# Kernel optimization log

Measured on AMD Instinct MI355X. Metric: run time of the kernel, lower is better.

## Reference

```python
import jax, jax.numpy as jnp
import numpy as np


def _apply_ry(state, theta, i, n):
    # state: [B, 2^n] complex; theta: scalar or [B]
    B = state.shape[0]
    s = state.reshape(B, 2**i, 2, 2**(n - i - 1))
    th = jnp.reshape(theta, (-1, 1, 1)) * 0.5
    c, sn = jnp.cos(th), jnp.sin(th)
    a0, a1 = s[:, :, 0], s[:, :, 1]
    return jnp.stack([c * a0 - sn * a1, sn * a0 + c * a1], axis=2).reshape(B, -1)


def _apply_rz(state, theta, i, n):
    B = state.shape[0]
    s = state.reshape(B, 2**i, 2, 2**(n - i - 1))
    ph = jnp.exp(-0.5j * jnp.reshape(theta, (-1, 1, 1)).astype(jnp.float32))
    return jnp.stack([s[:, :, 0] * ph, s[:, :, 1] * jnp.conj(ph)], axis=2).reshape(B, -1)


def _apply_cnot(state, c, t, n):
    # CNOT(control=c, target=t); flips target amplitudes on control=1 slice
    B = state.shape[0]
    s = state.reshape((B,) + (2,) * n)
    ax_c, ax_t = 1 + c, 1 + t
    zero = jnp.take(s, 0, axis=ax_c)
    one = jnp.take(s, 1, axis=ax_c)
    one = jnp.flip(one, axis=ax_t - (1 if t > c else 0))
    return jnp.stack([zero, one], axis=ax_c).reshape(B, -1)


def _z_signs(n):
    # signs[i, k] = +1 if bit i of basis index k is 0 else -1 (qubit 0 = MSB)
    idx = np.arange(2**n)
    bits = (idx[None, :] >> (n - 1 - np.arange(n))[:, None]) & 1
    return jnp.asarray(1.0 - 2.0 * bits, dtype=jnp.float32)  # [n, 2^n]


def _circuit(q_in, w_ry, w_rz):
    # Batched state-vector simulation of: AngleEmbedding(RY) ->
    # n_layers x (per-qubit RY,RZ + CNOT ring) -> <Z_i> expectations.
    B, n = q_in.shape
    L = w_ry.shape[0]
    state = jnp.zeros((B, 2**n), jnp.complex64).at[:, 0].set(1.0)
    for i in range(n):  # AngleEmbedding with rotation='Y'
        state = _apply_ry(state, q_in[:, i], i, n)
    for l in range(L):
        for i in range(n):
            state = _apply_ry(state, w_ry[l, i], i, n)
            state = _apply_rz(state, w_rz[l, i], i, n)
        for i in range(n):  # CNOT ring
            state = _apply_cnot(state, i, (i + 1) % n, n)
    probs = jnp.abs(state) ** 2  # [B, 2^n]
    return probs @ _z_signs(n).T  # [B, n] = <Z_i>


def setup_inputs():
    key = jax.random.key(0)
    ks = jax.random.split(key, 6)
    B, D, n, L = 4096, 512, 10, 4
    return {
        "x": jax.random.normal(ks[0], (B, D), jnp.float32),
        "pre_w": jax.random.normal(ks[1], (n, D), jnp.float32) / np.sqrt(D).astype(np.float32),
        "pre_b": jnp.zeros((n,), jnp.float32),
        "post_w": jax.random.normal(ks[2], (1, n), jnp.float32) / np.sqrt(n).astype(np.float32),
        "post_b": jnp.zeros((1,), jnp.float32),
        "w_ry": jax.random.normal(ks[3], (L, n), jnp.float32),
        "w_rz": jax.random.normal(ks[4], (L, n), jnp.float32),
    }


def reference(x, pre_w, pre_b, post_w, post_b, w_ry, w_rz):
    q_in = x @ pre_w.T + pre_b      # pre_net: [B, n_qubits] rotation angles
    z = _circuit(q_in, w_ry, w_rz)  # [B, n_qubits] PauliZ expectations
    return z @ post_w.T + post_b    # post_net: [B, 1] logits
```

## Files before the change

### kernel.cpp

```cpp
#include <hip/hip_runtime.h>

#define DEV static __device__ __forceinline__

template <int CTRL>
DEV float dpp_mov(float v) {
    int i = __float_as_int(v);
    i = __builtin_amdgcn_update_dpp(i, i, CTRL, 0xF, 0xF, false);
    return __int_as_float(i);
}
template <int PAT>
DEV float swz(float v) {
    return __int_as_float(__builtin_amdgcn_ds_swizzle(__float_as_int(v), PAT));
}
DEV float bperm(int byteaddr, float v) {
    return __int_as_float(__builtin_amdgcn_ds_bpermute(byteaddr, __float_as_int(v)));
}

#if __has_builtin(__builtin_amdgcn_permlane16_swap)
#define HAVE_PL16 1
DEV void pl16_pair(float v, float &r0, float &r1) {
    auto r = __builtin_amdgcn_permlane16_swap(__float_as_int(v), __float_as_int(v),
                                              false, false);
    r0 = __int_as_float((int)r[0]);
    r1 = __int_as_float((int)r[1]);
}
#endif
#if __has_builtin(__builtin_amdgcn_permlane32_swap)
#define HAVE_PL32 1
DEV void pl32_pair(float v, float &r0, float &r1) {
    auto r = __builtin_amdgcn_permlane32_swap(__float_as_int(v), __float_as_int(v),
                                              false, false);
    r0 = __int_as_float((int)r[0]);
    r1 = __int_as_float((int)r[1]);
}
#endif

DEV float wave_sum(float v, int a32) {
    v += dpp_mov<0xB1>(v);
    v += dpp_mov<0x4E>(v);
    v += dpp_mov<0x141>(v);
    v += dpp_mov<0x128>(v);
#ifdef HAVE_PL16
    {
        float r0, r1;
        pl16_pair(v, r0, r1);
        v = r0 + r1;
    }
#else
    v += swz<0x401F>(v);
#endif
#ifdef HAVE_PL32
    {
        float r0, r1;
        pl32_pair(v, r0, r1);
        v = r0 + r1;
    }
#else
    v += bperm(a32, v);
#endif
    return v;
}

template <int P>
DEV void apply_ry(float (&re)[16], float (&im)[16], float c, float s, int lane,
                  int a32, bool cv16, bool cv32) {
    if constexpr (P == 9) {
#ifdef HAVE_PL32
        const bool hi = (lane & 32) != 0;
        const float fl = hi ? s : c;
        const float fh = hi ? c : -s;
        const float g0 = cv32 ? fl : fh;
        const float g1 = cv32 ? fh : fl;
#pragma unroll
        for (int r = 0; r < 16; ++r) {
            float x0, x1, y0, y1;
            pl32_pair(re[r], x0, x1);
            pl32_pair(im[r], y0, y1);
            re[r] = fmaf(g0, x0, g1 * x1);
            im[r] = fmaf(g0, y0, g1 * y1);
        }
#else
        const float sg = (lane & 32) ? s : -s;
#pragma unroll
        for (int r = 0; r < 16; ++r) {
            float pr = bperm(a32, re[r]);
            float pi = bperm(a32, im[r]);
            re[r] = fmaf(c, re[r], sg * pr);
            im[r] = fmaf(c, im[r], sg * pi);
        }
#endif
    } else if constexpr (P == 8) {
#ifdef HAVE_PL16
        const bool hi = (lane & 16) != 0;
        const float fl = hi ? s : c;
        const float fh = hi ? c : -s;
        const float g0 = cv16 ? fl : fh;
        const float g1 = cv16 ? fh : fl;
#pragma unroll
        for (int r = 0; r < 16; ++r) {
            float x0, x1, y0, y1;
            pl16_pair(re[r], x0, x1);
            pl16_pair(im[r], y0, y1);
            re[r] = fmaf(g0, x0, g1 * x1);
            im[r] = fmaf(g0, y0, g1 * y1);
        }
#else
        const float sg = (lane & 16) ? s : -s;
#pragma unroll
        for (int r = 0; r < 16; ++r) {
            float pr = swz<0x401F>(re[r]);
            float pi = swz<0x401F>(im[r]);
            re[r] = fmaf(c, re[r], sg * pr);
            im[r] = fmaf(c, im[r], sg * pi);
        }
#endif
    } else if constexpr (P >= 4) {
        constexpr int mask = 1 << (P - 4);
        const float sg = (lane & mask) ? s : -s;
#pragma unroll
        for (int r = 0; r < 16; ++r) {
            float pr, pi;
            if constexpr (mask == 8) {
                pr = dpp_mov<0x128>(re[r]);
                pi = dpp_mov<0x128>(im[r]);
            } else if constexpr (mask == 4) {
                pr = dpp_mov<0x1B>(dpp_mov<0x141>(re[r]));
                pi = dpp_mov<0x1B>(dpp_mov<0x141>(im[r]));
            } else if constexpr (mask == 2) {
                pr = dpp_mov<0x4E>(re[r]);
                pi = dpp_mov<0x4E>(im[r]);
            } else {
                pr = dpp_mov<0xB1>(re[r]);
                pi = dpp_mov<0xB1>(im[r]);
            }
            re[r] = fmaf(c, re[r], sg * pr);
            im[r] = fmaf(c, im[r], sg * pi);
        }
    } else {
        constexpr int tb = 1 << P;
#pragma unroll
        for (int r = 0; r < 16; ++r) {
            if (!(r & tb)) {
                const int r2 = r | tb;
                float a0r = re[r], a1r = re[r2];
                float a0i = im[r], a1i = im[r2];
                re[r]  = fmaf(c, a0r, -s * a1r);
                re[r2] = fmaf(s, a0r,  c * a1r);
                im[r]  = fmaf(c, a0i, -s * a1i);
                im[r2] = fmaf(s, a0i,  c * a1i);
            }
        }
    }
}

DEV int g_of(int a) {
    a ^= ((a >> 1) & 1) ? 1 : 0;
    a ^= ((a >> 2) & 1) ? 2 : 0;
    a ^= ((a >> 3) & 1) ? 4 : 0;
    a ^= ((a >> 4) & 1) ? 8 : 0;
    a ^= ((a >> 5) & 1) ? 16 : 0;
    return a;
}

DEV void build_rz_tables(const float (&zc)[10], const float (&zs)[10], int lane,
                         float (&p67r)[4], float (&p67i)[4], float (&p89r)[4],
                         float (&p89i)[4]) {
    float plr, pli;
    pli = ((lane >> 5) & 1) ? zs[0] : -zs[0];
    plr = zc[0];
#pragma unroll
    for (int q = 1; q < 6; ++q) {
        float sq = ((lane >> (5 - q)) & 1) ? zs[q] : -zs[q];
        float nr = plr * zc[q] - pli * sq;
        float ni = plr * sq + pli * zc[q];
        plr = nr; pli = ni;
    }
    const float c6 = zc[6], s6 = zs[6], c7 = zc[7], s7 = zs[7];
    const float c8 = zc[8], s8 = zs[8], c9 = zc[9], s9 = zs[9];
#pragma unroll
    for (int j = 0; j < 4; ++j) {
        float sg6 = (j >> 1) ? s6 : -s6;
        float sg7 = (j & 1) ? s7 : -s7;
        float ar = c6 * c7 - sg6 * sg7;
        float ai = c6 * sg7 + sg6 * c7;
        p67r[j] = ar * plr - ai * pli;
        p67i[j] = ar * pli + ai * plr;
        float sg8 = (j >> 1) ? s8 : -s8;
        float sg9 = (j & 1) ? s9 : -s9;
        p89r[j] = c8 * c9 - sg8 * sg9;
        p89i[j] = c8 * sg9 + sg8 * c9;
    }
}

DEV void cnot_ring(float (&re)[16], float (&im)[16], int cA, int cB, int lane) {
#pragma unroll
    for (int r = 0; r < 16; ++r) {
        const int addr = ((0x6996 >> r) & 1) ? cB : cA;
        re[r] = bperm(addr, re[r]);
        im[r] = bperm(addr, im[r]);
    }
    {
        const bool ctrl = (lane & 1) != 0;
#pragma unroll
        for (int r = 0; r < 8; ++r) {
            const int r2 = r | 8;
            float t0 = re[r], t1 = re[r2];
            re[r]  = ctrl ? t1 : t0;
            re[r2] = ctrl ? t0 : t1;
            float u0 = im[r], u1 = im[r2];
            im[r]  = ctrl ? u1 : u0;
            im[r2] = ctrl ? u0 : u1;
        }
    }
#pragma unroll
    for (int r = 0; r < 16; ++r)
        if ((r & 8) && !(r & 4)) {
            const int r2 = r | 4;
            float t = re[r]; re[r] = re[r2]; re[r2] = t;
            t = im[r]; im[r] = im[r2]; im[r2] = t;
        }
#pragma unroll
    for (int r = 0; r < 16; ++r)
        if ((r & 4) && !(r & 2)) {
            const int r2 = r | 2;
            float t = re[r]; re[r] = re[r2]; re[r2] = t;
            t = im[r]; im[r] = im[r2]; im[r2] = t;
        }
#pragma unroll
    for (int r = 0; r < 16; ++r)
        if ((r & 2) && !(r & 1)) {
            const int r2 = r | 1;
            float t = re[r]; re[r] = re[r2]; re[r2] = t;
            t = im[r]; im[r] = im[r2]; im[r2] = t;
        }
}

__global__ __launch_bounds__(256, 4) void dqc_main_kernel(
    const float* __restrict__ x, const float* __restrict__ pre_w,
    const float* __restrict__ pre_b, const float* __restrict__ post_w,
    const float* __restrict__ post_b, const float* __restrict__ w_ry,
    const float* __restrict__ w_rz, float* __restrict__ out, int B) {
    __shared__ float2 sh_trig[80];
    {
        int t = threadIdx.x;
        if (t < 80) {
            float ang = (t < 40 ? w_ry[t] : w_rz[t - 40]) * 0.5f;
            float sv, cv;
            __sincosf(ang, &sv, &cv);
            sh_trig[t] = make_float2(cv, sv);
        }
    }
    __syncthreads();

    const int lane = threadIdx.x & 63;
    const int wid = threadIdx.x >> 6;
    const int b = blockIdx.x * 4 + wid;
    if (b >= B) return;

    const int a32 = (lane ^ 32) << 2;

    bool cv16 = false, cv32 = false;
#ifdef HAVE_PL16
    {
        auto r = __builtin_amdgcn_permlane16_swap(lane, lane, false, false);
        cv16 = ((int)r[0] == (lane & ~16));
    }
#endif
#ifdef HAVE_PL32
    {
        auto r = __builtin_amdgcn_permlane32_swap(lane, lane, false, false);
        cv32 = ((int)r[0] == (lane & ~32));
    }
#endif

    const int h0 = lane ^ ((lane & 1) ? 32 : 0);
    const int cA = g_of(h0) << 2;
    const int cB = g_of(h0 ^ 32) << 2;

    float th[10];
#pragma unroll
    for (int i = 0; i < 10; ++i) th[i] = 0.f;
    const float4* xb4 = reinterpret_cast<const float4*>(x + (size_t)b * 512);
    const float4* pw4 = reinterpret_cast<const float4*>(pre_w);
#pragma unroll
    for (int k = 0; k < 2; ++k) {
        const int idx = lane + 64 * k;
        const float4 xv = xb4[idx];
#pragma unroll
        for (int i = 0; i < 10; ++i) {
            const float4 wv = pw4[i * 128 + idx];
            th[i] = fmaf(xv.x, wv.x, th[i]);
            th[i] = fmaf(xv.y, wv.y, th[i]);
            th[i] = fmaf(xv.z, wv.z, th[i]);
            th[i] = fmaf(xv.w, wv.w, th[i]);
        }
    }
#pragma unroll
    for (int i = 0; i < 10; ++i) th[i] = wave_sum(th[i], a32) + pre_b[i];

    float f0r[10], f0i[10], f1r[10], f1i[10];
#pragma unroll
    for (int q = 0; q < 10; ++q) {
        float hh = 0.5f * (th[q] + w_ry[q]);
        float sh_, ch_;
        __sincosf(hh, &sh_, &ch_);
        float2 z = sh_trig[40 + q];
        f0r[q] = ch_ * z.x;  f0i[q] = -ch_ * z.y;
        f1r[q] = sh_ * z.x;  f1i[q] =  sh_ * z.y;
    }
    float Lr, Li;
    {
        int bq = (lane >> 5) & 1;
        Lr = bq ? f1r[0] : f0r[0];
        Li = bq ? f1i[0] : f0i[0];
#pragma unroll
        for (int q = 1; q < 6; ++q) {
            int bb = (lane >> (5 - q)) & 1;
            float br = bb ? f1r[q] : f0r[q];
            float bi = bb ? f1i[q] : f0i[q];
            float nr = Lr * br - Li * bi;
            float ni = Lr * bi + Li * br;
            Lr = nr; Li = ni;
        }
    }
    float t67r[4], t67i[4], t89r[4], t89i[4];
#pragma unroll
    for (int j = 0; j < 4; ++j) {
        float ar = (j >> 1) ? f1r[6] : f0r[6];
        float ai = (j >> 1) ? f1i[6] : f0i[6];
        float br = (j & 1) ? f1r[7] : f0r[7];
        float bi = (j & 1) ? f1i[7] : f0i[7];
        float pr = ar * br - ai * bi;
        float pi = ar * bi + ai * br;
        t67r[j] = pr * Lr - pi * Li;
        t67i[j] = pr * Li + pi * Lr;
        float cr_ = (j >> 1) ? f1r[8] : f0r[8];
        float ci_ = (j >> 1) ? f1i[8] : f0i[8];
        float dr = (j & 1) ? f1r[9] : f0r[9];
        float di = (j & 1) ? f1i[9] : f0i[9];
        t89r[j] = cr_ * dr - ci_ * di;
        t89i[j] = cr_ * di + ci_ * dr;
    }
    float re[16], im[16];
#pragma unroll
    for (int r = 0; r < 16; ++r) {
        const int j = r >> 2, k = r & 3;
        re[r] = t67r[j] * t89r[k] - t67i[j] * t89i[k];
        im[r] = t67r[j] * t89i[k] + t67i[j] * t89r[k];
    }
    cnot_ring(re, im, cA, cB, lane);

#pragma unroll 1
    for (int l = 1; l < 4; ++l) {
        float yc[10], ys[10], zc[10], zs[10];
#pragma unroll
        for (int q = 0; q < 10; ++q) {
            float2 v = sh_trig[l * 10 + q];
            yc[q] = v.x; ys[q] = v.y;
            float2 w = sh_trig[40 + l * 10 + q];
            zc[q] = w.x; zs[q] = w.y;
        }
        apply_ry<9>(re, im, yc[0], ys[0], lane, a32, cv16, cv32);
        apply_ry<8>(re, im, yc[1], ys[1], lane, a32, cv16, cv32);
        apply_ry<7>(re, im, yc[2], ys[2], lane, a32, cv16, cv32);
        apply_ry<6>(re, im, yc[3], ys[3], lane, a32, cv16, cv32);
        apply_ry<5>(re, im, yc[4], ys[4], lane, a32, cv16, cv32);
        apply_ry<4>(re, im, yc[5], ys[5], lane, a32, cv16, cv32);
        apply_ry<3>(re, im, yc[6], ys[6], lane, a32, cv16, cv32);
        apply_ry<2>(re, im, yc[7], ys[7], lane, a32, cv16, cv32);
        apply_ry<1>(re, im, yc[8], ys[8], lane, a32, cv16, cv32);
        apply_ry<0>(re, im, yc[9], ys[9], lane, a32, cv16, cv32);

        float p67r[4], p67i[4], p89r[4], p89i[4];
        build_rz_tables(zc, zs, lane, p67r, p67i, p89r, p89i);
#pragma unroll
        for (int r = 0; r < 16; ++r) {
            const int j = r >> 2, k = r & 3;
            float t_r = re[r] * p67r[j] - im[r] * p67i[j];
            float t_i = re[r] * p67i[j] + im[r] * p67r[j];
            re[r] = t_r * p89r[k] - t_i * p89i[k];
            im[r] = t_r * p89i[k] + t_i * p89r[k];
        }
        cnot_ring(re, im, cA, cB, lane);
    }

    float laneC = 0.f;
#pragma unroll
    for (int j = 0; j < 6; ++j) {
        int bit = (lane >> (5 - j)) & 1;
        laneC += post_w[j] * (1.f - 2.f * (float)bit);
    }
    const float w6 = post_w[6], w7 = post_w[7], w8 = post_w[8], w9 = post_w[9];
    float base67[4], m89[4];
#pragma unroll
    for (int j = 0; j < 4; ++j) {
        base67[j] = laneC + ((j >> 1) ? -w6 : w6) + ((j & 1) ? -w7 : w7);
        m89[j] = ((j >> 1) ? -w8 : w8) + ((j & 1) ? -w9 : w9);
    }
    float acc = 0.f;
#pragma unroll
    for (int r = 0; r < 16; ++r) {
        float p = fmaf(re[r], re[r], im[r] * im[r]);
        acc = fmaf(p, base67[r >> 2] + m89[r & 3], acc);
    }
    acc = wave_sum(acc, a32);
    if (lane == 0) out[b] = acc + post_b[0];
}

extern "C" void kernel_launch(void* const* d_in, const int* in_sizes, int n_in,
                              void* d_out, int out_size, void* d_ws, size_t ws_size,
                              hipStream_t stream) {
    const float* x      = (const float*)d_in[0];
    const float* pre_w  = (const float*)d_in[1];
    const float* pre_b  = (const float*)d_in[2];
    const float* post_w = (const float*)d_in[3];
    const float* post_b = (const float*)d_in[4];
    const float* w_ry   = (const float*)d_in[5];
    const float* w_rz   = (const float*)d_in[6];
    float* out = (float*)d_out;
    (void)d_ws; (void)ws_size;

    const int B = in_sizes[0] / 512;

    dqc_main_kernel<<<(B + 3) / 4, 256, 0, stream>>>(x, pre_w, pre_b, post_w,
                                                     post_b, w_ry, w_rz, out, B);
}
```

Measured before the change: 96.34 us.

## Process two batch samples per wavefront to interleave independent state-vector work

Each wavefront now simulates two batch rows at once, interleaving their gate applications, CNOT permutes and pre_w loads so the independent chains can hide cross-lane latency and share weight loads. The last layer's RZ and CNOT ring are skipped, and the readout coefficients are remapped to fold in that permutation, since those diagonal phases and permutations are absorbed by the final probability readout. Launch bounds drop to two blocks per CU and the grid halves, raising register pressure and lowering occupancy in exchange for more instruction-level parallelism.

```diff
diff --git a/kernel.cpp b/kernel.cpp
--- a/kernel.cpp
+++ b/kernel.cpp
@@ -192,119 +192,76 @@
     }
 }
 
-DEV void cnot_ring(float (&re)[16], float (&im)[16], int cA, int cB, int lane) {
+DEV void cnot_ring2(float (&reA)[16], float (&imA)[16], float (&reB)[16],
+                    float (&imB)[16], int cA_, int cB_, int lane) {
 #pragma unroll
     for (int r = 0; r < 16; ++r) {
-        const int addr = ((0x6996 >> r) & 1) ? cB : cA;
-        re[r] = bperm(addr, re[r]);
-        im[r] = bperm(addr, im[r]);
+        const int addr = ((0x6996 >> r) & 1) ? cB_ : cA_;
+        reA[r] = bperm(addr, reA[r]);
+        imA[r] = bperm(addr, imA[r]);
+        reB[r] = bperm(addr, reB[r]);
+        imB[r] = bperm(addr, imB[r]);
     }
     {
         const bool ctrl = (lane & 1) != 0;
 #pragma unroll
         for (int r = 0; r < 8; ++r) {
             const int r2 = r | 8;
-            float t0 = re[r], t1 = re[r2];
-            re[r]  = ctrl ? t1 : t0;
-            re[r2] = ctrl ? t0 : t1;
-            float u0 = im[r], u1 = im[r2];
-            im[r]  = ctrl ? u1 : u0;
-            im[r2] = ctrl ? u0 : u1;
+            float t0 = reA[r], t1 = reA[r2];
+            reA[r]  = ctrl ? t1 : t0;
+            reA[r2] = ctrl ? t0 : t1;
+            float u0 = imA[r], u1 = imA[r2];
+            imA[r]  = ctrl ? u1 : u0;
+            imA[r2] = ctrl ? u0 : u1;
+            float v0 = reB[r], v1 = reB[r2];
+            reB[r]  = ctrl ? v1 : v0;
+            reB[r2] = ctrl ? v0 : v1;
+            float w0 = imB[r], w1 = imB[r2];
+            imB[r]  = ctrl ? w1 : w0;
+            imB[r2] = ctrl ? w0 : w1;
         }
     }
 #pragma unroll
     for (int r = 0; r < 16; ++r)
         if ((r & 8) && !(r & 4)) {
             const int r2 = r | 4;
-            float t = re[r]; re[r] = re[r2]; re[r2] = t;
-            t = im[r]; im[r] = im[r2]; im[r2] = t;
+            float t;
+            t = reA[r]; reA[r] = reA[r2]; reA[r2] = t;
+            t = imA[r]; imA[r] = imA[r2]; imA[r2] = t;
+            t = reB[r]; reB[r] = reB[r2]; reB[r2] = t;
+            t = imB[r]; imB[r] = imB[r2]; imB[r2] = t;
         }
 #pragma unroll
     for (int r = 0; r < 16; ++r)
         if ((r & 4) && !(r & 2)) {
             const int r2 = r | 2;
-            float t = re[r]; re[r] = re[r2]; re[r2] = t;
-            t = im[r]; im[r] = im[r2]; im[r2] = t;
+            float t;
+            t = reA[r]; reA[r] = reA[r2]; reA[r2] = t;
+            t = imA[r]; imA[r] = imA[r2]; imA[r2] = t;
+            t = reB[r]; reB[r] = reB[r2]; reB[r2] = t;
+            t = imB[r]; imB[r] = imB[r2]; imB[r2] = t;
         }
 #pragma unroll
     for (int r = 0; r < 16; ++r)
         if ((r & 2) && !(r & 1)) {
             const int r2 = r | 1;
-            float t = re[r]; re[r] = re[r2]; re[r2] = t;
-            t = im[r]; im[r] = im[r2]; im[r2] = t;
-        }
-}
-
-__global__ __launch_bounds__(256, 4) void dqc_main_kernel(
-    const float* __restrict__ x, const float* __restrict__ pre_w,
-    const float* __restrict__ pre_b, const float* __restrict__ post_w,
-    const float* __restrict__ post_b, const float* __restrict__ w_ry,
-    const float* __restrict__ w_rz, float* __restrict__ out, int B) {
-    __shared__ float2 sh_trig[80];
-    {
-        int t = threadIdx.x;
-        if (t < 80) {
-            float ang = (t < 40 ? w_ry[t] : w_rz[t - 40]) * 0.5f;
-            float sv, cv;
-            __sincosf(ang, &sv, &cv);
-            sh_trig[t] = make_float2(cv, sv);
-        }
-    }
-    __syncthreads();
-
-    const int lane = threadIdx.x & 63;
-    const int wid = threadIdx.x >> 6;
-    const int b = blockIdx.x * 4 + wid;
-    if (b >= B) return;
-
-    const int a32 = (lane ^ 32) << 2;
-
-    bool cv16 = false, cv32 = false;
-#ifdef HAVE_PL16
-    {
-        auto r = __builtin_amdgcn_permlane16_swap(lane, lane, false, false);
-        cv16 = ((int)r[0] == (lane & ~16));
-    }
-#endif
-#ifdef HAVE_PL32
-    {
-        auto r = __builtin_amdgcn_permlane32_swap(lane, lane, false, false);
-        cv32 = ((int)r[0] == (lane & ~32));
-    }
-#endif
-
-    const int h0 = lane ^ ((lane & 1) ? 32 : 0);
-    const int cA = g_of(h0) << 2;
-    const int cB = g_of(h0 ^ 32) << 2;
-
-    float th[10];
-#pragma unroll
-    for (int i = 0; i < 10; ++i) th[i] = 0.f;
-    const float4* xb4 = reinterpret_cast<const float4*>(x + (size_t)b * 512);
-    const float4* pw4 = reinterpret_cast<const float4*>(pre_w);
-#pragma unroll
-    for (int k = 0; k < 2; ++k) {
-        const int idx = lane + 64 * k;
-        const float4 xv = xb4[idx];
-#pragma unroll
-        for (int i = 0; i < 10; ++i) {
-            const float4 wv = pw4[i * 128 + idx];
-            th[i] = fmaf(xv.x, wv.x, th[i]);
-            th[i] = fmaf(xv.y, wv.y, th[i]);
-            th[i] = fmaf(xv.z, wv.z, th[i]);
-            th[i] = fmaf(xv.w, wv.w, th[i]);
-        }
-    }
-#pragma unroll
-    for (int i = 0; i < 10; ++i) th[i] = wave_sum(th[i], a32) + pre_b[i];
-
+            float t;
+            t = reA[r]; reA[r] = reA[r2]; reA[r2] = t;
+            t = imA[r]; imA[r] = imA[r2]; imA[r2] = t;
+            t = reB[r]; reB[r] = reB[r2]; reB[r2] = t;
+            t = imB[r]; imB[r] = imB[r2]; imB[r2] = t;
+        }
+}
+
+DEV void fold0(const float (&th)[10], const float* __restrict__ w_ry,
+               const float2* shz, int lane, float (&re)[16], float (&im)[16]) {
     float f0r[10], f0i[10], f1r[10], f1i[10];
 #pragma unroll
     for (int q = 0; q < 10; ++q) {
         float hh = 0.5f * (th[q] + w_ry[q]);
         float sh_, ch_;
         __sincosf(hh, &sh_, &ch_);
-        float2 z = sh_trig[40 + q];
+        float2 z = shz[q];
         f0r[q] = ch_ * z.x;  f0i[q] = -ch_ * z.y;
         f1r[q] = sh_ * z.x;  f1i[q] =  sh_ * z.y;
     }
@@ -341,70 +298,177 @@
         t89r[j] = cr_ * dr - ci_ * di;
         t89i[j] = cr_ * di + ci_ * dr;
     }
-    float re[16], im[16];
 #pragma unroll
     for (int r = 0; r < 16; ++r) {
         const int j = r >> 2, k = r & 3;
         re[r] = t67r[j] * t89r[k] - t67i[j] * t89i[k];
         im[r] = t67r[j] * t89i[k] + t67i[j] * t89r[k];
     }
-    cnot_ring(re, im, cA, cB, lane);
+}
+
+__global__ __launch_bounds__(256, 2) void dqc_main_kernel(
+    const float* __restrict__ x, const float* __restrict__ pre_w,
+    const float* __restrict__ pre_b, const float* __restrict__ post_w,
+    const float* __restrict__ post_b, const float* __restrict__ w_ry,
+    const float* __restrict__ w_rz, float* __restrict__ out, int B) {
+    __shared__ float2 sh_trig[80];
+    {
+        int t = threadIdx.x;
+        if (t < 80) {
+            float ang = (t < 40 ? w_ry[t] : w_rz[t - 40]) * 0.5f;
+            float sv, cv;
+            __sincosf(ang, &sv, &cv);
+            sh_trig[t] = make_float2(cv, sv);
+        }
+    }
+    __syncthreads();
+
+    const int lane = threadIdx.x & 63;
+    const int wid = threadIdx.x >> 6;
+    const int b0 = (blockIdx.x * 4 + wid) * 2;
+    const int b1 = b0 + 1;
+    if (b0 >= B) return;
+
+    const int a32 = (lane ^ 32) << 2;
+
+    bool cv16 = false, cv32 = false;
+#ifdef HAVE_PL16
+    {
+        auto r = __builtin_amdgcn_permlane16_swap(lane, lane, false, false);
+        cv16 = ((int)r[0] == (lane & ~16));
+    }
+#endif
+#ifdef HAVE_PL32
+    {
+        auto r = __builtin_amdgcn_permlane32_swap(lane, lane, false, false);
+        cv32 = ((int)r[0] == (lane & ~32));
+    }
+#endif
+
+    const int h0 = lane ^ ((lane & 1) ? 32 : 0);
+    const int cA = g_of(h0) << 2;
+    const int cB = g_of(h0 ^ 32) << 2;
+
+    float thA[10], thB[10];
+#pragma unroll
+    for (int i = 0; i < 10; ++i) { thA[i] = 0.f; thB[i] = 0.f; }
+    const float4* xA4 = reinterpret_cast<const float4*>(x + (size_t)b0 * 512);
+    const float4* xB4 = reinterpret_cast<const float4*>(x + (size_t)b1 * 512);
+    const float4* pw4 = reinterpret_cast<const float4*>(pre_w);
+    const bool haveB = (b1 < B);
+#pragma unroll
+    for (int k = 0; k < 2; ++k) {
+        const int idx = lane + 64 * k;
+        const float4 xa = xA4[idx];
+        const float4 xb = haveB ? xB4[idx] : xa;
+#pragma unroll
+        for (int i = 0; i < 10; ++i) {
+            const float4 wv = pw4[i * 128 + idx];
+            thA[i] = fmaf(xa.x, wv.x, thA[i]);
+            thA[i] = fmaf(xa.y, wv.y, thA[i]);
+            thA[i] = fmaf(xa.z, wv.z, thA[i]);
+            thA[i] = fmaf(xa.w, wv.w, thA[i]);
+            thB[i] = fmaf(xb.x, wv.x, thB[i]);
+            thB[i] = fmaf(xb.y, wv.y, thB[i]);
+            thB[i] = fmaf(xb.z, wv.z, thB[i]);
+            thB[i] = fmaf(xb.w, wv.w, thB[i]);
+        }
+    }
+#pragma unroll
+    for (int i = 0; i < 10; ++i) {
+        thA[i] = wave_sum(thA[i], a32) + pre_b[i];
+        thB[i] = wave_sum(thB[i], a32) + pre_b[i];
+    }
+
+    float reA[16], imA[16], reB[16], imB[16];
+    fold0(thA, w_ry, sh_trig + 40, lane, reA, imA);
+    fold0(thB, w_ry, sh_trig + 40, lane, reB, imB);
+    cnot_ring2(reA, imA, reB, imB, cA, cB, lane);
 
 #pragma unroll 1
     for (int l = 1; l < 4; ++l) {
-        float yc[10], ys[10], zc[10], zs[10];
+        float yc[10], ys[10];
 #pragma unroll
         for (int q = 0; q < 10; ++q) {
             float2 v = sh_trig[l * 10 + q];
             yc[q] = v.x; ys[q] = v.y;
-            float2 w = sh_trig[40 + l * 10 + q];
-            zc[q] = w.x; zs[q] = w.y;
-        }
-        apply_ry<9>(re, im, yc[0], ys[0], lane, a32, cv16, cv32);
-        apply_ry<8>(re, im, yc[1], ys[1], lane, a32, cv16, cv32);
-        apply_ry<7>(re, im, yc[2], ys[2], lane, a32, cv16, cv32);
-        apply_ry<6>(re, im, yc[3], ys[3], lane, a32, cv16, cv32);
-        apply_ry<5>(re, im, yc[4], ys[4], lane, a32, cv16, cv32);
-        apply_ry<4>(re, im, yc[5], ys[5], lane, a32, cv16, cv32);
-        apply_ry<3>(re, im, yc[6], ys[6], lane, a32, cv16, cv32);
-        apply_ry<2>(re, im, yc[7], ys[7], lane, a32, cv16, cv32);
-        apply_ry<1>(re, im, yc[8], ys[8], lane, a32, cv16, cv32);
-        apply_ry<0>(re, im, yc[9], ys[9], lane, a32, cv16, cv32);
-
-        float p67r[4], p67i[4], p89r[4], p89i[4];
-        build_rz_tables(zc, zs, lane, p67r, p67i, p89r, p89i);
-#pragma unroll
-        for (int r = 0; r < 16; ++r) {
-            const int j = r >> 2, k = r & 3;
-            float t_r = re[r] * p67r[j] - im[r] * p67i[j];
-            float t_i = re[r] * p67i[j] + im[r] * p67r[j];
-            re[r] = t_r * p89r[k] - t_i * p89i[k];
-            im[r] = t_r * p89i[k] + t_i * p89r[k];
-        }
-        cnot_ring(re, im, cA, cB, lane);
-    }
-
-    float laneC = 0.f;
-#pragma unroll
-    for (int j = 0; j < 6; ++j) {
-        int bit = (lane >> (5 - j)) & 1;
-        laneC += post_w[j] * (1.f - 2.f * (float)bit);
-    }
+        }
+        apply_ry<9>(reA, imA, yc[0], ys[0], lane, a32, cv16, cv32);
+        apply_ry<9>(reB, imB, yc[0], ys[0], lane, a32, cv16, cv32);
+        apply_ry<8>(reA, imA, yc[1], ys[1], lane, a32, cv16, cv32);
+        apply_ry<8>(reB, imB, yc[1], ys[1], lane, a32, cv16, cv32);
+        apply_ry<7>(reA, imA, yc[2], ys[2], lane, a32, cv16, cv32);
+        apply_ry<7>(reB, imB, yc[2], ys[2], lane, a32, cv16, cv32);
+        apply_ry<6>(reA, imA, yc[3], ys[3], lane, a32, cv16, cv32);
+        apply_ry<6>(reB, imB, yc[3], ys[3], lane, a32, cv16, cv32);
+        apply_ry<5>(reA, imA, yc[4], ys[4], lane, a32, cv16, cv32);
+        apply_ry<5>(reB, imB, yc[4], ys[4], lane, a32, cv16, cv32);
+        apply_ry<4>(reA, imA, yc[5], ys[5], lane, a32, cv16, cv32);
+        apply_ry<4>(reB, imB, yc[5], ys[5], lane, a32, cv16, cv32);
+        apply_ry<3>(reA, imA, yc[6], ys[6], lane, a32, cv16, cv32);
+        apply_ry<3>(reB, imB, yc[6], ys[6], lane, a32, cv16, cv32);
+        apply_ry<2>(reA, imA, yc[7], ys[7], lane, a32, cv16, cv32);
+        apply_ry<2>(reB, imB, yc[7], ys[7], lane, a32, cv16, cv32);
+        apply_ry<1>(reA, imA, yc[8], ys[8], lane, a32, cv16, cv32);
+        apply_ry<1>(reB, imB, yc[8], ys[8], lane, a32, cv16, cv32);
+        apply_ry<0>(reA, imA, yc[9], ys[9], lane, a32, cv16, cv32);
+        apply_ry<0>(reB, imB, yc[9], ys[9], lane, a32, cv16, cv32);
+
+        if (l < 3) {
+            float zc[10], zs[10];
+#pragma unroll
+            for (int q = 0; q < 10; ++q) {
+                float2 w = sh_trig[40 + l * 10 + q];
+                zc[q] = w.x; zs[q] = w.y;
+            }
+            float p67r[4], p67i[4], p89r[4], p89i[4];
+            build_rz_tables(zc, zs, lane, p67r, p67i, p89r, p89i);
+#pragma unroll
+            for (int r = 0; r < 16; ++r) {
+                const int j = r >> 2, k = r & 3;
+                float t_r = reA[r] * p67r[j] - imA[r] * p67i[j];
+                float t_i = reA[r] * p67i[j] + imA[r] * p67r[j];
+                reA[r] = t_r * p89r[k] - t_i * p89i[k];
+                imA[r] = t_r * p89i[k] + t_i * p89r[k];
+                float u_r = reB[r] * p67r[j] - imB[r] * p67i[j];
+                float u_i = reB[r] * p67i[j] + imB[r] * p67r[j];
+                reB[r] = u_r * p89r[k] - u_i * p89i[k];
+                imB[r] = u_r * p89i[k] + u_i * p89r[k];
+            }
+            cnot_ring2(reA, imA, reB, imB, cA, cB, lane);
+        }
+    }
+
+    float A_lane = 0.f;
+    float L = ((lane >> 5) & 1) ? -1.f : 1.f;
+#pragma unroll
+    for (int j = 1; j <= 5; ++j) {
+        L = ((lane >> (5 - j)) & 1) ? -L : L;
+        A_lane += post_w[j] * L;
+    }
+    const float t0 = post_w[0] * (((lane >> 5) & 1) ? -L : L);
+    const float Ap = A_lane + t0, Am = A_lane - t0;
     const float w6 = post_w[6], w7 = post_w[7], w8 = post_w[8], w9 = post_w[9];
-    float base67[4], m89[4];
-#pragma unroll
-    for (int j = 0; j < 4; ++j) {
-        base67[j] = laneC + ((j >> 1) ? -w6 : w6) + ((j & 1) ? -w7 : w7);
-        m89[j] = ((j >> 1) ? -w8 : w8) + ((j & 1) ? -w9 : w9);
-    }
-    float acc = 0.f;
+    float accA = 0.f, accB = 0.f;
 #pragma unroll
     for (int r = 0; r < 16; ++r) {
-        float p = fmaf(re[r], re[r], im[r] * im[r]);
-        acc = fmaf(p, base67[r >> 2] + m89[r & 3], acc);
-    }
-    acc = wave_sum(acc, a32);
-    if (lane == 0) out[b] = acc + post_b[0];
+        float u = (r & 1) ? w8 - w9 : w8 + w9;
+        float v = (r & 2) ? w7 - u : w7 + u;
+        float wv = (r & 4) ? w6 - v : w6 + v;
+        float WR = (r & 8) ? -wv : wv;
+        const float base = ((0x6996 >> r) & 1) ? Am : Ap;
+        float coef = fmaf(L, WR, base);
+        float pA = fmaf(reA[r], reA[r], imA[r] * imA[r]);
+        accA = fmaf(pA, coef, accA);
+        float pB = fmaf(reB[r], reB[r], imB[r] * imB[r]);
+        accB = fmaf(pB, coef, accB);
+    }
+    accA = wave_sum(accA, a32);
+    accB = wave_sum(accB, a32);
+    if (lane == 0) {
+        out[b0] = accA + post_b[0];
+        if (haveB) out[b1] = accB + post_b[0];
+    }
 }
 
 extern "C" void kernel_launch(void* const* d_in, const int* in_sizes, int n_in,
@@ -421,7 +485,7 @@
     (void)d_ws; (void)ws_size;
 
     const int B = in_sizes[0] / 512;
-
-    dqc_main_kernel<<<(B + 3) / 4, 256, 0, stream>>>(x, pre_w, pre_b, post_w,
-                                                     post_b, w_ry, w_rz, out, B);
-}
+    const int waves = (B + 1) / 2;
+    dqc_main_kernel<<<(waves + 3) / 4, 256, 0, stream>>>(
+        x, pre_w, pre_b, post_w, post_b, w_ry, w_rz, out, B);
+}
```

Result: no change. 96.61 us (+0.3%).

## Process two batch samples per wave using packed fp32 FMA

Applied to the files above, without the earlier changes.

Each wave now simulates two batch samples at once, holding amplitudes as float2 vectors so arithmetic can map to packed FP32 FMA instructions. The shuffle work of permlane, DPP and bpermute is still issued per component, so only the ALU cost is amortized. The final layer's RZ and CNOT ring are skipped because they do not change Z-expectation probabilities, and the post-net coefficient computation is restructured. Register pressure doubles, so launch bounds drop from 4 to 2 waves per SIMD and half as many waves are launched, which reduces occupancy and latency hiding.

```diff
diff --git a/kernel.cpp b/kernel.cpp
--- a/kernel.cpp
+++ b/kernel.cpp
@@ -1,6 +1,11 @@
 #include <hip/hip_runtime.h>
 
 #define DEV static __device__ __forceinline__
+
+typedef float f2 __attribute__((ext_vector_type(2)));
+
+DEV f2 pkfma(f2 a, f2 b, f2 c) { return __builtin_elementwise_fma(a, b, c); }
+DEV f2 bc(float v) { return (f2){v, v}; }
 
 template <int CTRL>
 DEV float dpp_mov(float v) {
@@ -14,6 +19,14 @@
 }
 DEV float bperm(int byteaddr, float v) {
     return __int_as_float(__builtin_amdgcn_ds_bpermute(byteaddr, __float_as_int(v)));
+}
+
+template <int CTRL>
+DEV f2 dpp2(f2 v) { return (f2){dpp_mov<CTRL>(v.x), dpp_mov<CTRL>(v.y)}; }
+template <int PAT>
+DEV f2 swz2(f2 v) { return (f2){swz<PAT>(v.x), swz<PAT>(v.y)}; }
+DEV f2 bperm2(int addr, f2 v) {
+    return (f2){bperm(addr, v.x), bperm(addr, v.y)};
 }
 
 #if __has_builtin(__builtin_amdgcn_permlane16_swap)
@@ -24,6 +37,13 @@
     r0 = __int_as_float((int)r[0]);
     r1 = __int_as_float((int)r[1]);
 }
+DEV void pl16_pair2(f2 v, f2 &r0, f2 &r1) {
+    float a0, a1, b0, b1;
+    pl16_pair(v.x, a0, a1);
+    pl16_pair(v.y, b0, b1);
+    r0 = (f2){a0, b0};
+    r1 = (f2){a1, b1};
+}
 #endif
 #if __has_builtin(__builtin_amdgcn_permlane32_swap)
 #define HAVE_PL32 1
@@ -33,60 +53,68 @@
     r0 = __int_as_float((int)r[0]);
     r1 = __int_as_float((int)r[1]);
 }
-#endif
-
-DEV float wave_sum(float v, int a32) {
-    v += dpp_mov<0xB1>(v);
-    v += dpp_mov<0x4E>(v);
-    v += dpp_mov<0x141>(v);
-    v += dpp_mov<0x128>(v);
+DEV void pl32_pair2(f2 v, f2 &r0, f2 &r1) {
+    float a0, a1, b0, b1;
+    pl32_pair(v.x, a0, a1);
+    pl32_pair(v.y, b0, b1);
+    r0 = (f2){a0, b0};
+    r1 = (f2){a1, b1};
+}
+#endif
+
+DEV f2 wave_sum2(f2 v, int a32) {
+    v += dpp2<0xB1>(v);
+    v += dpp2<0x4E>(v);
+    v += dpp2<0x141>(v);
+    v += dpp2<0x128>(v);
 #ifdef HAVE_PL16
     {
-        float r0, r1;
-        pl16_pair(v, r0, r1);
+        f2 r0, r1;
+        pl16_pair2(v, r0, r1);
         v = r0 + r1;
     }
 #else
-    v += swz<0x401F>(v);
+    v += swz2<0x401F>(v);
 #endif
 #ifdef HAVE_PL32
     {
-        float r0, r1;
-        pl32_pair(v, r0, r1);
+        f2 r0, r1;
+        pl32_pair2(v, r0, r1);
         v = r0 + r1;
     }
 #else
-    v += bperm(a32, v);
+    v += bperm2(a32, v);
 #endif
     return v;
 }
 
 template <int P>
-DEV void apply_ry(float (&re)[16], float (&im)[16], float c, float s, int lane,
-                  int a32, bool cv16, bool cv32) {
+DEV void apply_ry2(f2 (&re)[16], f2 (&im)[16], float c, float s, int lane,
+                   int a32, bool cv16, bool cv32) {
     if constexpr (P == 9) {
 #ifdef HAVE_PL32
         const bool hi = (lane & 32) != 0;
         const float fl = hi ? s : c;
         const float fh = hi ? c : -s;
-        const float g0 = cv32 ? fl : fh;
-        const float g1 = cv32 ? fh : fl;
-#pragma unroll
-        for (int r = 0; r < 16; ++r) {
-            float x0, x1, y0, y1;
-            pl32_pair(re[r], x0, x1);
-            pl32_pair(im[r], y0, y1);
-            re[r] = fmaf(g0, x0, g1 * x1);
-            im[r] = fmaf(g0, y0, g1 * y1);
+        const f2 g0 = bc(cv32 ? fl : fh);
+        const f2 g1 = bc(cv32 ? fh : fl);
+#pragma unroll
+        for (int r = 0; r < 16; ++r) {
+            f2 x0, x1, y0, y1;
+            pl32_pair2(re[r], x0, x1);
+            pl32_pair2(im[r], y0, y1);
+            re[r] = pkfma(g0, x0, g1 * x1);
+            im[r] = pkfma(g0, y0, g1 * y1);
         }
 #else
-        const float sg = (lane & 32) ? s : -s;
-#pragma unroll
-        for (int r = 0; r < 16; ++r) {
-            float pr = bperm(a32, re[r]);
-            float pi = bperm(a32, im[r]);
-            re[r] = fmaf(c, re[r], sg * pr);
-            im[r] = fmaf(c, im[r], sg * pi);
+        const f2 sg = bc((lane & 32) ? s : -s);
+        const f2 cc = bc(c);
+#pragma unroll
+        for (int r = 0; r < 16; ++r) {
+            f2 pr = bperm2(a32, re[r]);
+            f2 pi = bperm2(a32, im[r]);
+            re[r] = pkfma(cc, re[r], sg * pr);
+            im[r] = pkfma(cc, im[r], sg * pi);
         }
 #endif
     } else if constexpr (P == 8) {
@@ -94,60 +122,65 @@
         const bool hi = (lane & 16) != 0;
         const float fl = hi ? s : c;
         const float fh = hi ? c : -s;
-        const float g0 = cv16 ? fl : fh;
-        const float g1 = cv16 ? fh : fl;
-#pragma unroll
-        for (int r = 0; r < 16; ++r) {
-            float x0, x1, y0, y1;
-            pl16_pair(re[r], x0, x1);
-            pl16_pair(im[r], y0, y1);
-            re[r] = fmaf(g0, x0, g1 * x1);
-            im[r] = fmaf(g0, y0, g1 * y1);
+        const f2 g0 = bc(cv16 ? fl : fh);
+        const f2 g1 = bc(cv16 ? fh : fl);
+#pragma unroll
+        for (int r = 0; r < 16; ++r) {
+            f2 x0, x1, y0, y1;
+            pl16_pair2(re[r], x0, x1);
+            pl16_pair2(im[r], y0, y1);
+            re[r] = pkfma(g0, x0, g1 * x1);
+            im[r] = pkfma(g0, y0, g1 * y1);
         }
 #else
-        const float sg = (lane & 16) ? s : -s;
-#pragma unroll
-        for (int r = 0; r < 16; ++r) {
-            float pr = swz<0x401F>(re[r]);
-            float pi = swz<0x401F>(im[r]);
-            re[r] = fmaf(c, re[r], sg * pr);
-            im[r] = fmaf(c, im[r], sg * pi);
+        const f2 sg = bc((lane & 16) ? s : -s);
+        const f2 cc = bc(c);
+#pragma unroll
+        for (int r = 0; r < 16; ++r) {
+            f2 pr = swz2<0x401F>(re[r]);
+            f2 pi = swz2<0x401F>(im[r]);
+            re[r] = pkfma(cc, re[r], sg * pr);
+            im[r] = pkfma(cc, im[r], sg * pi);
         }
 #endif
     } else if constexpr (P >= 4) {
         constexpr int mask = 1 << (P - 4);
-        const float sg = (lane & mask) ? s : -s;
-#pragma unroll
-        for (int r = 0; r < 16; ++r) {
-            float pr, pi;
+        const f2 sg = bc((lane & mask) ? s : -s);
+        const f2 cc = bc(c);
+#pragma unroll
+        for (int r = 0; r < 16; ++r) {
+            f2 pr, pi;
             if constexpr (mask == 8) {
-                pr = dpp_mov<0x128>(re[r]);
-                pi = dpp_mov<0x128>(im[r]);
+                pr = dpp2<0x128>(re[r]);
+                pi = dpp2<0x128>(im[r]);
             } else if constexpr (mask == 4) {
-                pr = dpp_mov<0x1B>(dpp_mov<0x141>(re[r]));
-                pi = dpp_mov<0x1B>(dpp_mov<0x141>(im[r]));
+                pr = dpp2<0x1B>(dpp2<0x141>(re[r]));
+                pi = dpp2<0x1B>(dpp2<0x141>(im[r]));
             } else if constexpr (mask == 2) {
-                pr = dpp_mov<0x4E>(re[r]);
-                pi = dpp_mov<0x4E>(im[r]);
+                pr = dpp2<0x4E>(re[r]);
+                pi = dpp2<0x4E>(im[r]);
             } else {
-                pr = dpp_mov<0xB1>(re[r]);
-                pi = dpp_mov<0xB1>(im[r]);
+                pr = dpp2<0xB1>(re[r]);
+                pi = dpp2<0xB1>(im[r]);
             }
-            re[r] = fmaf(c, re[r], sg * pr);
-            im[r] = fmaf(c, im[r], sg * pi);
+            re[r] = pkfma(cc, re[r], sg * pr);
+            im[r] = pkfma(cc, im[r], sg * pi);
         }
     } else {
         constexpr int tb = 1 << P;
+        const f2 cc = bc(c);
+        const f2 ss = bc(s);
+        const f2 ms = bc(-s);
 #pragma unroll
         for (int r = 0; r < 16; ++r) {
             if (!(r & tb)) {
                 const int r2 = r | tb;
-                float a0r = re[r], a1r = re[r2];
-                float a0i = im[r], a1i = im[r2];
-                re[r]  = fmaf(c, a0r, -s * a1r);
-                re[r2] = fmaf(s, a0r,  c * a1r);
-                im[r]  = fmaf(c, a0i, -s * a1i);
-                im[r2] = fmaf(s, a0i,  c * a1i);
+                f2 a0r = re[r], a1r = re[r2];
+                f2 a0i = im[r], a1i = im[r2];
+                re[r]  = pkfma(cc, a0r, ms * a1r);
+                re[r2] = pkfma(ss, a0r, cc * a1r);
+                im[r]  = pkfma(cc, a0i, ms * a1i);
+                im[r2] = pkfma(ss, a0i, cc * a1i);
             }
         }
     }
@@ -162,9 +195,9 @@
     return a;
 }
 
-DEV void build_rz_tables(const float (&zc)[10], const float (&zs)[10], int lane,
-                         float (&p67r)[4], float (&p67i)[4], float (&p89r)[4],
-                         float (&p89i)[4]) {
+DEV void build_rz_tables_pk(const float (&zc)[10], const float (&zs)[10],
+                            int lane, f2 (&p67r)[4], f2 (&p67i)[4],
+                            f2 (&p89r)[4], f2 (&p89i)[4]) {
     float plr, pli;
     pli = ((lane >> 5) & 1) ? zs[0] : -zs[0];
     plr = zc[0];
@@ -183,31 +216,31 @@
         float sg7 = (j & 1) ? s7 : -s7;
         float ar = c6 * c7 - sg6 * sg7;
         float ai = c6 * sg7 + sg6 * c7;
-        p67r[j] = ar * plr - ai * pli;
-        p67i[j] = ar * pli + ai * plr;
+        p67r[j] = bc(ar * plr - ai * pli);
+        p67i[j] = bc(ar * pli + ai * plr);
         float sg8 = (j >> 1) ? s8 : -s8;
         float sg9 = (j & 1) ? s9 : -s9;
-        p89r[j] = c8 * c9 - sg8 * sg9;
-        p89i[j] = c8 * sg9 + sg8 * c9;
-    }
-}
-
-DEV void cnot_ring(float (&re)[16], float (&im)[16], int cA, int cB, int lane) {
+        p89r[j] = bc(c8 * c9 - sg8 * sg9);
+        p89i[j] = bc(c8 * sg9 + sg8 * c9);
+    }
+}
+
+DEV void cnot_ring_pk(f2 (&re)[16], f2 (&im)[16], int cA_, int cB_, int lane) {
 #pragma unroll
     for (int r = 0; r < 16; ++r) {
-        const int addr = ((0x6996 >> r) & 1) ? cB : cA;
-        re[r] = bperm(addr, re[r]);
-        im[r] = bperm(addr, im[r]);
+        const int addr = ((0x6996 >> r) & 1) ? cB_ : cA_;
+        re[r] = bperm2(addr, re[r]);
+        im[r] = bperm2(addr, im[r]);
     }
     {
         const bool ctrl = (lane & 1) != 0;
 #pragma unroll
         for (int r = 0; r < 8; ++r) {
             const int r2 = r | 8;
-            float t0 = re[r], t1 = re[r2];
+            f2 t0 = re[r], t1 = re[r2];
             re[r]  = ctrl ? t1 : t0;
             re[r2] = ctrl ? t0 : t1;
-            float u0 = im[r], u1 = im[r2];
+            f2 u0 = im[r], u1 = im[r2];
             im[r]  = ctrl ? u1 : u0;
             im[r2] = ctrl ? u0 : u1;
         }
@@ -216,26 +249,84 @@
     for (int r = 0; r < 16; ++r)
         if ((r & 8) && !(r & 4)) {
             const int r2 = r | 4;
-            float t = re[r]; re[r] = re[r2]; re[r2] = t;
+            f2 t;
+            t = re[r]; re[r] = re[r2]; re[r2] = t;
             t = im[r]; im[r] = im[r2]; im[r2] = t;
         }
 #pragma unroll
     for (int r = 0; r < 16; ++r)
         if ((r & 4) && !(r & 2)) {
             const int r2 = r | 2;
-            float t = re[r]; re[r] = re[r2]; re[r2] = t;
+            f2 t;
+            t = re[r]; re[r] = re[r2]; re[r2] = t;
             t = im[r]; im[r] = im[r2]; im[r2] = t;
         }
 #pragma unroll
     for (int r = 0; r < 16; ++r)
         if ((r & 2) && !(r & 1)) {
             const int r2 = r | 1;
-            float t = re[r]; re[r] = re[r2]; re[r2] = t;
+            f2 t;
+            t = re[r]; re[r] = re[r2]; re[r2] = t;
             t = im[r]; im[r] = im[r2]; im[r2] = t;
         }
 }
 
-__global__ __launch_bounds__(256, 4) void dqc_main_kernel(
+DEV void fold0_pk(const f2 (&th)[10], const float* __restrict__ w_ry,
+                  const float2* shz, int lane, f2 (&re)[16], f2 (&im)[16]) {
+    f2 f0r[10], f0i[10], f1r[10], f1i[10];
+#pragma unroll
+    for (int q = 0; q < 10; ++q) {
+        f2 hh = (th[q] + bc(w_ry[q])) * bc(0.5f);
+        float sA, cA, sB, cB;
+        __sincosf(hh.x, &sA, &cA);
+        __sincosf(hh.y, &sB, &cB);
+        f2 ch = (f2){cA, cB}, sh = (f2){sA, sB};
+        float2 z = shz[q];
+        f0r[q] = ch * bc(z.x);  f0i[q] = ch * bc(-z.y);
+        f1r[q] = sh * bc(z.x);  f1i[q] = sh * bc(z.y);
+    }
+    f2 Lr, Li;
+    {
+        int bq = (lane >> 5) & 1;
+        Lr = bq ? f1r[0] : f0r[0];
+        Li = bq ? f1i[0] : f0i[0];
+#pragma unroll
+        for (int q = 1; q < 6; ++q) {
+            int bb = (lane >> (5 - q)) & 1;
+            f2 br = bb ? f1r[q] : f0r[q];
+            f2 bi = bb ? f1i[q] : f0i[q];
+            f2 nr = pkfma(Li, -bi, Lr * br);
+            f2 ni = pkfma(Li, br, Lr * bi);
+            Lr = nr; Li = ni;
+        }
+    }
+    f2 t67r[4], t67i[4], t89r[4], t89i[4];
+#pragma unroll
+    for (int j = 0; j < 4; ++j) {
+        f2 ar = (j >> 1) ? f1r[6] : f0r[6];
+        f2 ai = (j >> 1) ? f1i[6] : f0i[6];
+        f2 br = (j & 1) ? f1r[7] : f0r[7];
+        f2 bi = (j & 1) ? f1i[7] : f0i[7];
+        f2 pr = pkfma(ai, -bi, ar * br);
+        f2 pi = pkfma(ai, br, ar * bi);
+        t67r[j] = pkfma(pi, -Li, pr * Lr);
+        t67i[j] = pkfma(pi, Lr, pr * Li);
+        f2 cr_ = (j >> 1) ? f1r[8] : f0r[8];
+        f2 ci_ = (j >> 1) ? f1i[8] : f0i[8];
+        f2 dr = (j & 1) ? f1r[9] : f0r[9];
+        f2 di = (j & 1) ? f1i[9] : f0i[9];
+        t89r[j] = pkfma(ci_, -di, cr_ * dr);
+        t89i[j] = pkfma(ci_, dr, cr_ * di);
+    }
+#pragma unroll
+    for (int r = 0; r < 16; ++r) {
+        const int j = r >> 2, k = r & 3;
+        re[r] = pkfma(t67i[j], -t89i[k], t67r[j] * t89r[k]);
+        im[r] = pkfma(t67i[j], t89r[k], t67r[j] * t89i[k]);
+    }
+}
+
+__global__ __launch_bounds__(256, 2) void dqc_main_kernel(
     const float* __restrict__ x, const float* __restrict__ pre_w,
     const float* __restrict__ pre_b, const float* __restrict__ post_w,
     const float* __restrict__ post_b, const float* __restrict__ w_ry,
@@ -254,8 +345,9 @@
 
     const int lane = threadIdx.x & 63;
     const int wid = threadIdx.x >> 6;
-    const int b = blockIdx.x * 4 + wid;
-    if (b >= B) return;
+    const int b0 = (blockIdx.x * 4 + wid) * 2;
+    const int b1 = b0 + 1;
+    if (b0 >= B) return;
 
     const int a32 = (lane ^ 32) << 2;
 
@@ -277,134 +369,105 @@
     const int cA = g_of(h0) << 2;
     const int cB = g_of(h0 ^ 32) << 2;
 
-    float th[10];
-#pragma unroll
-    for (int i = 0; i < 10; ++i) th[i] = 0.f;
-    const float4* xb4 = reinterpret_cast<const float4*>(x + (size_t)b * 512);
+    f2 th[10];
+#pragma unroll
+    for (int i = 0; i < 10; ++i) th[i] = (f2){0.f, 0.f};
+    const float4* xA4 = reinterpret_cast<const float4*>(x + (size_t)b0 * 512);
+    const float4* xB4 = reinterpret_cast<const float4*>(x + (size_t)b1 * 512);
     const float4* pw4 = reinterpret_cast<const float4*>(pre_w);
+    const bool haveB = (b1 < B);
 #pragma unroll
     for (int k = 0; k < 2; ++k) {
         const int idx = lane + 64 * k;
-        const float4 xv = xb4[idx];
+        const float4 xa = xA4[idx];
+        const float4 xb = haveB ? xB4[idx] : xa;
+        const f2 xp0 = (f2){xa.x, xb.x};
+        const f2 xp1 = (f2){xa.y, xb.y};
+        const f2 xp2 = (f2){xa.z, xb.z};
+        const f2 xp3 = (f2){xa.w, xb.w};
 #pragma unroll
         for (int i = 0; i < 10; ++i) {
             const float4 wv = pw4[i * 128 + idx];
-            th[i] = fmaf(xv.x, wv.x, th[i]);
-            th[i] = fmaf(xv.y, wv.y, th[i]);
-            th[i] = fmaf(xv.z, wv.z, th[i]);
-            th[i] = fmaf(xv.w, wv.w, th[i]);
-        }
-    }
-#pragma unroll
-    for (int i = 0; i < 10; ++i) th[i] = wave_sum(th[i], a32) + pre_b[i];
-
-    float f0r[10], f0i[10], f1r[10], f1i[10];
-#pragma unroll
-    for (int q = 0; q < 10; ++q) {
-        float hh = 0.5f * (th[q] + w_ry[q]);
-        float sh_, ch_;
-        __sincosf(hh, &sh_, &ch_);
-        float2 z = sh_trig[40 + q];
-        f0r[q] = ch_ * z.x;  f0i[q] = -ch_ * z.y;
-        f1r[q] = sh_ * z.x;  f1i[q] =  sh_ * z.y;
-    }
-    float Lr, Li;
-    {
-        int bq = (lane >> 5) & 1;
-        Lr = bq ? f1r[0] : f0r[0];
-        Li = bq ? f1i[0] : f0i[0];
-#pragma unroll
-        for (int q = 1; q < 6; ++q) {
-            int bb = (lane >> (5 - q)) & 1;
-            float br = bb ? f1r[q] : f0r[q];
-            float bi = bb ? f1i[q] : f0i[q];
-            float nr = Lr * br - Li * bi;
-            float ni = Lr * bi + Li * br;
-            Lr = nr; Li = ni;
-        }
-    }
-    float t67r[4], t67i[4], t89r[4], t89i[4];
-#pragma unroll
-    for (int j = 0; j < 4; ++j) {
-        float ar = (j >> 1) ? f1r[6] : f0r[6];
-        float ai = (j >> 1) ? f1i[6] : f0i[6];
-        float br = (j & 1) ? f1r[7] : f0r[7];
-        float bi = (j & 1) ? f1i[7] : f0i[7];
-        float pr = ar * br - ai * bi;
-        float pi = ar * bi + ai * br;
-        t67r[j] = pr * Lr - pi * Li;
-        t67i[j] = pr * Li + pi * Lr;
-        float cr_ = (j >> 1) ? f1r[8] : f0r[8];
-        float ci_ = (j >> 1) ? f1i[8] : f0i[8];
-        float dr = (j & 1) ? f1r[9] : f0r[9];
-        float di = (j & 1) ? f1i[9] : f0i[9];
-        t89r[j] = cr_ * dr - ci_ * di;
-        t89i[j] = cr_ * di + ci_ * dr;
-    }
-    float re[16], im[16];
-#pragma unroll
-    for (int r = 0; r < 16; ++r) {
-        const int j = r >> 2, k = r & 3;
-        re[r] = t67r[j] * t89r[k] - t67i[j] * t89i[k];
-        im[r] = t67r[j] * t89i[k] + t67i[j] * t89r[k];
-    }
-    cnot_ring(re, im, cA, cB, lane);
+            th[i] = pkfma(xp0, bc(wv.x), th[i]);
+            th[i] = pkfma(xp1, bc(wv.y), th[i]);
+            th[i] = pkfma(xp2, bc(wv.z), th[i]);
+            th[i] = pkfma(xp3, bc(wv.w), th[i]);
+        }
+    }
+#pragma unroll
+    for (int i = 0; i < 10; ++i) th[i] = wave_sum2(th[i], a32) + bc(pre_b[i]);
+
+    f2 re[16], im[16];
+    fold0_pk(th, w_ry, sh_trig + 40, lane, re, im);
+    cnot_ring_pk(re, im, cA, cB, lane);
 
 #pragma unroll 1
     for (int l = 1; l < 4; ++l) {
-        float yc[10], ys[10], zc[10], zs[10];
+        float yc[10], ys[10];
 #pragma unroll
         for (int q = 0; q < 10; ++q) {
             float2 v = sh_trig[l * 10 + q];
             yc[q] = v.x; ys[q] = v.y;
-            float2 w = sh_trig[40 + l * 10 + q];
-            zc[q] = w.x; zs[q] = w.y;
-        }
-        apply_ry<9>(re, im, yc[0], ys[0], lane, a32, cv16, cv32);
-        apply_ry<8>(re, im, yc[1], ys[1], lane, a32, cv16, cv32);
-        apply_ry<7>(re, im, yc[2], ys[2], lane, a32, cv16, cv32);
-        apply_ry<6>(re, im, yc[3], ys[3], lane, a32, cv16, cv32);
-        apply_ry<5>(re, im, yc[4], ys[4], lane, a32, cv16, cv32);
-        apply_ry<4>(re, im, yc[5], ys[5], lane, a32, cv16, cv32);
-        apply_ry<3>(re, im, yc[6], ys[6], lane, a32, cv16, cv32);
-        apply_ry<2>(re, im, yc[7], ys[7], lane, a32, cv16, cv32);
-        apply_ry<1>(re, im, yc[8], ys[8], lane, a32, cv16, cv32);
-        apply_ry<0>(re, im, yc[9], ys[9], lane, a32, cv16, cv32);
-
-        float p67r[4], p67i[4], p89r[4], p89i[4];
-        build_rz_tables(zc, zs, lane, p67r, p67i, p89r, p89i);
-#pragma unroll
-        for (int r = 0; r < 16; ++r) {
-            const int j = r >> 2, k = r & 3;
-            float t_r = re[r] * p67r[j] - im[r] * p67i[j];
-            float t_i = re[r] * p67i[j] + im[r] * p67r[j];
-            re[r] = t_r * p89r[k] - t_i * p89i[k];
-            im[r] = t_r * p89i[k] + t_i * p89r[k];
-        }
-        cnot_ring(re, im, cA, cB, lane);
-    }
-
-    float laneC = 0.f;
-#pragma unroll
-    for (int j = 0; j < 6; ++j) {
-        int bit = (lane >> (5 - j)) & 1;
-        laneC += post_w[j] * (1.f - 2.f * (float)bit);
-    }
+        }
+        apply_ry2<9>(re, im, yc[0], ys[0], lane, a32, cv16, cv32);
+        apply_ry2<8>(re, im, yc[1], ys[1], lane, a32, cv16, cv32);
+        apply_ry2<7>(re, im, yc[2], ys[2], lane, a32, cv16, cv32);
+        apply_ry2<6>(re, im, yc[3], ys[3], lane, a32, cv16, cv32);
+        apply_ry2<5>(re, im, yc[4], ys[4], lane, a32, cv16, cv32);
+        apply_ry2<4>(re, im, yc[5], ys[5], lane, a32, cv16, cv32);
+        apply_ry2<3>(re, im, yc[6], ys[6], lane, a32, cv16, cv32);
+        apply_ry2<2>(re, im, yc[7], ys[7], lane, a32, cv16, cv32);
+        apply_ry2<1>(re, im, yc[8], ys[8], lane, a32, cv16, cv32);
+        apply_ry2<0>(re, im, yc[9], ys[9], lane, a32, cv16, cv32);
+
+        if (l < 3) {
+            float zc[10], zs[10];
+#pragma unroll
+            for (int q = 0; q < 10; ++q) {
+                float2 w = sh_trig[40 + l * 10 + q];
+                zc[q] = w.x; zs[q] = w.y;
+            }
+            f2 p67r[4], p67i[4], p89r[4], p89i[4];
+            build_rz_tables_pk(zc, zs, lane, p67r, p67i, p89r, p89i);
+#pragma unroll
+            for (int r = 0; r < 16; ++r) {
+                const int j = r >> 2, k = r & 3;
+                f2 t_r = pkfma(im[r], -p67i[j], re[r] * p67r[j]);
+                f2 t_i = pkfma(im[r], p67r[j], re[r] * p67i[j]);
+                re[r] = pkfma(t_i, -p89i[k], t_r * p89r[k]);
+                im[r] = pkfma(t_i, p89r[k], t_r * p89i[k]);
+            }
+            cnot_ring_pk(re, im, cA, cB, lane);
+        }
+    }
+
+    float A_lane = 0.f;
+    float L = ((lane >> 5) & 1) ? -1.f : 1.f;
+#pragma unroll
+    for (int j = 1; j <= 5; ++j) {
+        L = ((lane >> (5 - j)) & 1) ? -L : L;
+        A_lane += post_w[j] * L;
+    }
+    const float t0 = post_w[0] * (((lane >> 5) & 1) ? -L : L);
+    const float Ap = A_lane + t0, Am = A_lane - t0;
     const float w6 = post_w[6], w7 = post_w[7], w8 = post_w[8], w9 = post_w[9];
-    float base67[4], m89[4];
-#pragma unroll
-    for (int j = 0; j < 4; ++j) {
-        base67[j] = laneC + ((j >> 1) ? -w6 : w6) + ((j & 1) ? -w7 : w7);
-        m89[j] = ((j >> 1) ? -w8 : w8) + ((j & 1) ? -w9 : w9);
-    }
-    float acc = 0.f;
+    f2 acc = (f2){0.f, 0.f};
 #pragma unroll
     for (int r = 0; r < 16; ++r) {
-        float p = fmaf(re[r], re[r], im[r] * im[r]);
-        acc = fmaf(p, base67[r >> 2] + m89[r & 3], acc);
-    }
-    acc = wave_sum(acc, a32);
-    if (lane == 0) out[b] = acc + post_b[0];
+        float u = (r & 1) ? w8 - w9 : w8 + w9;
+        float v = (r & 2) ? w7 - u : w7 + u;
+        float wv = (r & 4) ? w6 - v : w6 + v;
+        float WR = (r & 8) ? -wv : wv;
+        const float base = ((0x6996 >> r) & 1) ? Am : Ap;
+        float coef = fmaf(L, WR, base);
+        f2 p = pkfma(re[r], re[r], im[r] * im[r]);
+        acc = pkfma(p, bc(coef), acc);
+    }
+    acc = wave_sum2(acc, a32);
+    if (lane == 0) {
+        out[b0] = acc.x + post_b[0];
+        if (haveB) out[b1] = acc.y + post_b[0];
+    }
 }
 
 extern "C" void kernel_launch(void* const* d_in, const int* in_sizes, int n_in,
@@ -421,7 +484,7 @@
     (void)d_ws; (void)ws_size;
 
     const int B = in_sizes[0] / 512;
-
-    dqc_main_kernel<<<(B + 3) / 4, 256, 0, stream>>>(x, pre_w, pre_b, post_w,
-                                                     post_b, w_ry, w_rz, out, B);
-}
+    const int waves = (B + 1) / 2;
+    dqc_main_kernel<<<(waves + 3) / 4, 256, 0, stream>>>(
+        x, pre_w, pre_b, post_w, post_b, w_ry, w_rz, out, B);
+}
```

New measurement: 95.19 us. Within noise of the previous version (-1.2%).
